# Performance work log

Measured on AMD Instinct MI355X. Metric: run time of the kernel, lower is better.

## Reference

```python
import jax, jax.numpy as jnp
import numpy as np

B, C, F_IN = 262144, 4, 4   # batch, num label nodes, feature dim
HID = 64                     # hidden_dim (MLP embedding dim / GCN input)
GCN_H, GCN_OUT = 32, 4
EPS = 1e-8                   # torch F.cosine_similarity eps


def _glorot(k, shape):
    lim = float(np.sqrt(6.0 / (shape[0] + shape[1])))
    return jax.random.uniform(k, shape, jnp.float32, -lim, lim)


def setup_inputs() -> dict:
    key = jax.random.key(0)
    ks = jax.random.split(key, 7)
    return dict(
        x=jax.random.normal(ks[0], (B, C, F_IN), jnp.float32),
        # LabelEmbeddingMLP: 4 -> 128 -> 64 -> HID
        W1=_glorot(ks[1], (F_IN, 128)), b1=jnp.zeros((128,), jnp.float32),
        W2=_glorot(ks[2], (128, 64)),   b2=jnp.zeros((64,), jnp.float32),
        W3=_glorot(ks[3], (64, HID)),   b3=jnp.zeros((HID,), jnp.float32),
        # GCNModel: GCNConv(HID,32) -> GCNConv(32,4)
        Wg1=_glorot(ks[4], (HID, GCN_H)), bg1=jnp.zeros((GCN_H,), jnp.float32),
        Wg2=_glorot(ks[5], (GCN_H, GCN_OUT)), bg2=jnp.zeros((GCN_OUT,), jnp.float32),
    )


def reference(x, W1, b1, W2, b2, W3, b3, Wg1, bg1, Wg2, bg2):
    # --- label embedding MLP (applied per node) ---
    h = jax.nn.relu(x @ W1 + b1)
    h = jax.nn.relu(h @ W2 + b2)
    emb = h @ W3 + b3                                    # [B, C, HID]

    # --- per-sample cosine similarity, thresholded, unioned over batch ---
    # (the torch code keeps adding edges to ONE nx.Graph across all k, so the
    #  resulting 4-node edge set is the union over the batch; edge weights are
    #  ignored because GCNConv is called without edge_weight)
    n = x / jnp.maximum(jnp.linalg.norm(x, axis=-1, keepdims=True), EPS)
    sim = jnp.einsum('bif,bjf->bij', n, n)               # [B, C, C]
    adj = (sim > 0.5).any(axis=0) & ~jnp.eye(C, dtype=bool)
    adj = adj | adj.T

    # --- GCN normalized adjacency with self-loops: D^-1/2 (A+I) D^-1/2 ---
    A = adj.astype(jnp.float32) + jnp.eye(C, dtype=jnp.float32)
    dinv = jax.lax.rsqrt(A.sum(axis=1))
    Ahat = jax.lax.stop_gradient(dinv[:, None] * A * dinv[None, :])  # graph built via .item() is detached in torch

    # --- two GCNConv layers, shared Ahat broadcast over batch ---
    g = jax.nn.relu(jnp.einsum('ij,bjh->bih', Ahat, emb @ Wg1) + bg1)  # [B, C, 32]
    out = jnp.einsum('ij,bjh->bih', Ahat, g @ Wg2) + bg2               # [B, C, 4]
    return emb, out
```

## Files before the change

### kernel.cpp

```cpp
#include <hip/hip_runtime.h>

#define NB 262144
#define NNODE (NB * 4)
#define EMB_ELEMS ((size_t)NNODE * 64)
#define ADJ_BLOCKS (NNODE / 256)

typedef __attribute__((ext_vector_type(8))) _Float16 f16x8;
typedef __attribute__((ext_vector_type(4))) float f32x4;
typedef __attribute__((ext_vector_type(4))) unsigned int u32x4;

#define OW1E  0
#define OW2T  10240
#define OW3T  27648
#define OW3GT 36864
#define OF32  41472
#define IMG_BYTES 42880
#define FB2   0
#define FB3   64
#define FB3G  128
#define FBG1  160
#define FWG2  192
#define FBG2  320
#define FAHAT 324

#define NWAVE 8
#define SB_STRIDE 36
#define WBUF_BYTES (64 * SB_STRIDE * 2)
#define SMEM_BYTES (IMG_BYTES + NWAVE * WBUF_BYTES)

template <int J>
__device__ __forceinline__ float qb(float v) {
    constexpr int ctrl = J | (J << 2) | (J << 4) | (J << 6);
    int r = __builtin_amdgcn_update_dpp(0, __builtin_bit_cast(int, v), ctrl, 0xF, 0xF, true);
    return __builtin_bit_cast(float, r);
}

__device__ __forceinline__ float sum_xor16(float u) {
    float a = u, b = u;
    asm("v_permlane16_swap_b32 %0, %1" : "+v"(a), "+v"(b));
    return a + b;
}
__device__ __forceinline__ float sum_xor32(float u) {
    float a = u, b = u;
    asm("v_permlane32_swap_b32 %0, %1" : "+v"(a), "+v"(b));
    return a + b;
}

__global__ __launch_bounds__(256) void adj_kernel(const float* __restrict__ x,
                                                  unsigned int* __restrict__ mask_arr) {
    __shared__ unsigned int smask;
    if (threadIdx.x == 0) smask = 0u;
    __syncthreads();

    const int t = blockIdx.x * 256 + threadIdx.x;
    const int c = t & 3;
    f32x4 v = *(const f32x4*)(x + (size_t)t * 4);
    float nn = sqrtf(v.x * v.x + v.y * v.y + v.z * v.z + v.w * v.w);
    float inv = 1.0f / fmaxf(nn, 1e-8f);

    unsigned int m = 0u;
#define DOTJ(J) do {                                                            \
        const float bx = qb<J>(v.x), by = qb<J>(v.y);                           \
        const float bz = qb<J>(v.z), bw = qb<J>(v.w);                           \
        const float bi = qb<J>(inv);                                            \
        const float d = v.x * bx + v.y * by + v.z * bz + v.w * bw;              \
        if ((int)((J) != c) & (int)(d * inv * bi > 0.5f)) {                     \
            const int i_ = c < (J) ? c : (J);                                   \
            const int j_ = c < (J) ? (J) : c;                                   \
            m |= 1u << (2 * i_ + j_ - 1 - (i_ >> 1));                           \
        }                                                                       \
    } while (0)
    DOTJ(0); DOTJ(1); DOTJ(2); DOTJ(3);
#undef DOTJ

    if (m) atomicOr(&smask, m);
    __syncthreads();
    if (threadIdx.x == 0) mask_arr[blockIdx.x] = smask;
}

__global__ __launch_bounds__(256) void prep_kernel(
    const float* __restrict__ W1, const float* __restrict__ b1,
    const float* __restrict__ W2, const float* __restrict__ b2,
    const float* __restrict__ W3, const float* __restrict__ b3,
    const float* __restrict__ Wg1, const float* __restrict__ bg1,
    const float* __restrict__ Wg2, const float* __restrict__ bg2,
    const unsigned int* __restrict__ mask_arr, char* __restrict__ img)
{
    const int t = threadIdx.x;
    const int bid = blockIdx.x;
    _Float16* H = (_Float16*)img;
    float* F = (float*)(img + OF32);

    if (bid == 0) {
        __shared__ unsigned red[256];
        unsigned um = 0u;
        for (int i = t; i < ADJ_BLOCKS; i += 256) um |= mask_arr[i];
        red[t] = um;
        __syncthreads();
        for (int s = 128; s > 0; s >>= 1) {
            if (t < s) red[t] |= red[t + s];
            __syncthreads();
        }
        const unsigned m = red[0];

        for (int i = t; i < 64; i += 256) F[FB2 + i] = b2[i];
        for (int i = t; i < 64; i += 256) F[FB3 + i] = b3[i];
        for (int i = t; i < 32; i += 256) {
            float s = 0.f;
            for (int h = 0; h < 64; ++h) s = fmaf(b3[h], Wg1[h * 32 + i], s);
            F[FB3G + i] = s;
        }
        for (int i = t; i < 32; i += 256) F[FBG1 + i] = bg1[i];
        for (int i = t; i < 128; i += 256) F[FWG2 + i] = Wg2[i];
        for (int i = t; i < 4; i += 256) F[FBG2 + i] = bg2[i];
        if (t == 0) {
            float A[4][4];
            for (int i = 0; i < 4; ++i)
                for (int j = 0; j < 4; ++j) A[i][j] = (i == j) ? 1.f : 0.f;
            int bit = 0;
            for (int i = 0; i < 4; ++i)
                for (int j = i + 1; j < 4; ++j) {
                    if ((m >> bit) & 1u) { A[i][j] = 1.f; A[j][i] = 1.f; }
                    ++bit;
                }
            float dinv[4];
            for (int i = 0; i < 4; ++i)
                dinv[i] = 1.0f / sqrtf(A[i][0] + A[i][1] + A[i][2] + A[i][3]);
            for (int i = 0; i < 4; ++i)
                for (int j = 0; j < 4; ++j) F[FAHAT + i * 4 + j] = dinv[i] * A[i][j] * dinv[j];
        }
    } else if (bid == 1) {
        for (int i = t; i < 128 * 40; i += 256) {
            int j = i / 40, kk = i % 40;
            float v = (kk < 4) ? W1[kk * 128 + j] : (kk == 4 ? b1[j] : 0.f);
            H[OW1E / 2 + i] = (_Float16)v;
        }
    } else if (bid == 2) {
        for (int i = t; i < 64 * 136; i += 256) {
            int jo = i / 136, ji = i % 136;
            H[OW2T / 2 + i] = (_Float16)(ji < 128 ? W2[ji * 64 + jo] : 0.f);
        }
    } else {
        for (int i = t; i < 64 * 72; i += 256) {
            int h = i / 72, j = i % 72;
            H[OW3T / 2 + i] = (_Float16)(j < 64 ? W3[j * 64 + h] : 0.f);
        }
        for (int i = t; i < 32 * 72; i += 256) {
            int e = i / 72, j = i % 72;
            float s = 0.f;
            if (j < 64)
                for (int h = 0; h < 64; ++h) s = fmaf(W3[j * 64 + h], Wg1[h * 32 + e], s);
            H[OW3GT / 2 + i] = (_Float16)s;
        }
    }
}

__device__ __forceinline__ unsigned pkf16(float a, float b) {
    unsigned short ha = __builtin_bit_cast(unsigned short, (_Float16)a);
    unsigned short hb = __builtin_bit_cast(unsigned short, (_Float16)b);
    return (unsigned)ha | ((unsigned)hb << 16);
}
__device__ __forceinline__ f32x4 MF(f16x8 a, f16x8 b, f32x4 c) {
    return __builtin_amdgcn_mfma_f32_16x16x32_f16(a, b, c, 0, 0, 0);
}
__device__ __forceinline__ f16x8 ldA(const _Float16* p) {
    return *(const f16x8*)p;
}

__global__ __launch_bounds__(512, 2) void mlp_gcn_mfma(
    const float* __restrict__ x, const char* __restrict__ img,
    float* __restrict__ emb_out, float* __restrict__ out_out)
{
    __shared__ u32x4 smem4[SMEM_BYTES / 16];
    char* smem = (char*)smem4;
    const int tx = threadIdx.x;
    {
        const u32x4* src = (const u32x4*)img;
        u32x4* dst = (u32x4*)smem;
        for (int i = tx; i < IMG_BYTES / 16; i += 512) dst[i] = src[i];
    }
    __syncthreads();

    const _Float16* wh = (const _Float16*)smem;
    const float* wf = (const float*)(smem + OF32);

    const int wid = tx >> 6, lane = tx & 63;
    const int g = lane >> 4, c = lane & 15;
    const bool g0 = (g == 0);

    char* wb = smem + IMG_BYTES + wid * WBUF_BYTES;
    _Float16* sb = (_Float16*)wb;
    float* tb = (float*)wb;

    const f32x4 arow = *(const f32x4*)(wf + FAHAT + (c & 3) * 4);
    f32x4 bg1v[2];
    bg1v[0] = *(const f32x4*)(wf + FBG1 + g * 4);
    bg1v[1] = *(const f32x4*)(wf + FBG1 + 16 + g * 4);
    const f32x4 bg2v = *(const f32x4*)(wf + FBG2);
    f32x4 wg2v[2][4];
#pragma unroll
    for (int m = 0; m < 2; ++m)
#pragma unroll
        for (int r = 0; r < 4; ++r)
            wg2v[m][r] = *(const f32x4*)(wf + FWG2 + (m * 16 + g * 4 + r) * 4);

    const size_t nbase0 = ((size_t)blockIdx.x * NWAVE + wid) * 128;
    f32x4 xv = *(const f32x4*)(x + (nbase0 + lane) * 4);

#pragma unroll 1
    for (int it = 0; it < 2; ++it) {
        const size_t nbase = nbase0 + (size_t)it * 64;
        const size_t pn = (it < 1) ? (nbase + 64) : nbase;
        f32x4 xnext = *(const f32x4*)(x + (pn + lane) * 4);

        {
            uint2 w0; w0.x = pkf16(xv.x, xv.y); w0.y = pkf16(xv.z, xv.w);
            uint2 w1; w1.x = 0x00003C00u; w1.y = 0u;
            *(uint2*)(sb + lane * SB_STRIDE + 0) = w0;
            *(uint2*)(sb + lane * SB_STRIDE + 4) = w1;
        }
        f16x8 xB[4];
#pragma unroll
        for (int nt = 0; nt < 4; ++nt) {
            uint2 lo = *(const uint2*)(sb + (nt * 16 + c) * SB_STRIDE + 0);
            uint2 hi = *(const uint2*)(sb + (nt * 16 + c) * SB_STRIDE + 4);
            u32x4 t;
            t.x = g0 ? lo.x : 0u; t.y = g0 ? lo.y : 0u;
            t.z = g0 ? hi.x : 0u; t.w = 0u;
            xB[nt] = __builtin_bit_cast(f16x8, t);
        }

        f32x4 acc2[4][4];
#pragma unroll
        for (int mt = 0; mt < 4; ++mt) {
            f32x4 bv = *(const f32x4*)(wf + FB2 + mt * 16 + g * 4);
#pragma unroll
            for (int nt = 0; nt < 4; ++nt) acc2[mt][nt] = bv;
        }
#pragma unroll
        for (int kt = 0; kt < 4; ++kt) {
#pragma unroll
            for (int mt2 = 0; mt2 < 2; ++mt2) {
                const int mt = 2 * kt + mt2;
                f16x8 a = ldA(wh + OW1E / 2 + (mt * 16 + c) * 40 + g * 8);
#pragma unroll
                for (int nt = 0; nt < 4; ++nt) {
                    f32x4 z = {0.f, 0.f, 0.f, 0.f};
                    f32x4 t = MF(a, xB[nt], z);
                    uint2 w;
                    w.x = pkf16(fmaxf(t[0], 0.f), fmaxf(t[1], 0.f));
                    w.y = pkf16(fmaxf(t[2], 0.f), fmaxf(t[3], 0.f));
                    *(uint2*)(sb + (nt * 16 + c) * SB_STRIDE + mt2 * 16 + g * 4) = w;
                }
            }
            f16x8 bf[4];
#pragma unroll
            for (int nt = 0; nt < 4; ++nt) {
                uint2 lo = *(const uint2*)(sb + (nt * 16 + c) * SB_STRIDE + g * 8);
                uint2 hi = *(const uint2*)(sb + (nt * 16 + c) * SB_STRIDE + g * 8 + 4);
                u32x4 t; t.x = lo.x; t.y = lo.y; t.z = hi.x; t.w = hi.y;
                bf[nt] = __builtin_bit_cast(f16x8, t);
            }
#pragma unroll
            for (int mt = 0; mt < 4; ++mt) {
                f16x8 a = ldA(wh + OW2T / 2 + (mt * 16 + c) * 136 + kt * 32 + g * 8);
#pragma unroll
                for (int nt = 0; nt < 4; ++nt) acc2[mt][nt] = MF(a, bf[nt], acc2[mt][nt]);
            }
        }

        unsigned pk2a[4][4][2];
#pragma unroll
        for (int mt = 0; mt < 4; ++mt)
#pragma unroll
            for (int nt = 0; nt < 4; ++nt) {
                pk2a[mt][nt][0] = pkf16(fmaxf(acc2[mt][nt][0], 0.f), fmaxf(acc2[mt][nt][1], 0.f));
                pk2a[mt][nt][1] = pkf16(fmaxf(acc2[mt][nt][2], 0.f), fmaxf(acc2[mt][nt][3], 0.f));
            }

        f32x4 acc3[4][4], acc4[2][4];
#pragma unroll
        for (int mt = 0; mt < 4; ++mt) {
            f32x4 bv = *(const f32x4*)(wf + FB3 + mt * 16 + g * 4);
#pragma unroll
            for (int nt = 0; nt < 4; ++nt) acc3[mt][nt] = bv;
        }
#pragma unroll
        for (int mt = 0; mt < 2; ++mt) {
            f32x4 bv = *(const f32x4*)(wf + FB3G + mt * 16 + g * 4);
#pragma unroll
            for (int nt = 0; nt < 4; ++nt) acc4[mt][nt] = bv;
        }
#pragma unroll
        for (int kt = 0; kt < 2; ++kt) {
#pragma unroll
            for (int mt2 = 0; mt2 < 2; ++mt2) {
                const int mt = 2 * kt + mt2;
#pragma unroll
                for (int nt = 0; nt < 4; ++nt) {
                    uint2 w; w.x = pk2a[mt][nt][0]; w.y = pk2a[mt][nt][1];
                    *(uint2*)(sb + (nt * 16 + c) * SB_STRIDE + mt2 * 16 + g * 4) = w;
                }
            }
            f16x8 bf[4];
#pragma unroll
            for (int nt = 0; nt < 4; ++nt) {
                uint2 lo = *(const uint2*)(sb + (nt * 16 + c) * SB_STRIDE + g * 8);
                uint2 hi = *(const uint2*)(sb + (nt * 16 + c) * SB_STRIDE + g * 8 + 4);
                u32x4 t; t.x = lo.x; t.y = lo.y; t.z = hi.x; t.w = hi.y;
                bf[nt] = __builtin_bit_cast(f16x8, t);
            }
#pragma unroll
            for (int mt = 0; mt < 4; ++mt) {
                f16x8 a = ldA(wh + OW3T / 2 + (mt * 16 + c) * 72 + kt * 32 + g * 8);
#pragma unroll
                for (int nt = 0; nt < 4; ++nt) acc3[mt][nt] = MF(a, bf[nt], acc3[mt][nt]);
            }
#pragma unroll
            for (int mt = 0; mt < 2; ++mt) {
                f16x8 a = ldA(wh + OW3GT / 2 + (mt * 16 + c) * 72 + kt * 32 + g * 8);
#pragma unroll
                for (int nt = 0; nt < 4; ++nt) acc4[mt][nt] = MF(a, bf[nt], acc4[mt][nt]);
            }
        }

#pragma unroll
        for (int nt = 0; nt < 4; ++nt) {
#pragma unroll
            for (int mt = 0; mt < 4; ++mt) {
                int sl = (mt * 4 + g) ^ (c & 7);
                *(f32x4*)(tb + c * 64 + sl * 4) = acc3[mt][nt];
            }
            float* gp = emb_out + (nbase + nt * 16) * 64;
#pragma unroll
            for (int s = 0; s < 4; ++s) {
                int row = s * 4 + g;
                int sl = c ^ (row & 7);
                f32x4 q = *(const f32x4*)(tb + row * 64 + sl * 4);
                *(f32x4*)(gp + s * 256 + lane * 4) = q;
            }
        }

#pragma unroll
        for (int nt = 0; nt < 4; ++nt) {
            float u[4] = {0.f, 0.f, 0.f, 0.f};
#pragma unroll
            for (int m = 0; m < 2; ++m)
#pragma unroll
                for (int r = 0; r < 4; ++r) {
                    float v = acc4[m][nt][r];
                    float s = bg1v[m][r];
                    s = fmaf(arow.x, qb<0>(v), s);
                    s = fmaf(arow.y, qb<1>(v), s);
                    s = fmaf(arow.z, qb<2>(v), s);
                    s = fmaf(arow.w, qb<3>(v), s);
                    s = fmaxf(s, 0.f);
                    u[0] = fmaf(s, wg2v[m][r].x, u[0]);
                    u[1] = fmaf(s, wg2v[m][r].y, u[1]);
                    u[2] = fmaf(s, wg2v[m][r].z, u[2]);
                    u[3] = fmaf(s, wg2v[m][r].w, u[3]);
                }
#pragma unroll
            for (int o = 0; o < 4; ++o)
                u[o] = sum_xor32(sum_xor16(u[o]));
            float ov[4];
#pragma unroll
            for (int o = 0; o < 4; ++o) {
                float s = bg2v[o];
                s = fmaf(arow.x, qb<0>(u[o]), s);
                s = fmaf(arow.y, qb<1>(u[o]), s);
                s = fmaf(arow.z, qb<2>(u[o]), s);
                s = fmaf(arow.w, qb<3>(u[o]), s);
                ov[o] = s;
            }
            if (g0) {
                f32x4 t; t.x = ov[0]; t.y = ov[1]; t.z = ov[2]; t.w = ov[3];
                *(f32x4*)(out_out + (nbase + nt * 16 + c) * 4) = t;
            }
        }

        xv = xnext;
    }
}

extern "C" void kernel_launch(void* const* d_in, const int* in_sizes, int n_in,
                              void* d_out, int out_size, void* d_ws, size_t ws_size,
                              hipStream_t stream) {
    const float* x   = (const float*)d_in[0];
    const float* W1  = (const float*)d_in[1];
    const float* b1  = (const float*)d_in[2];
    const float* W2  = (const float*)d_in[3];
    const float* b2  = (const float*)d_in[4];
    const float* W3  = (const float*)d_in[5];
    const float* b3  = (const float*)d_in[6];
    const float* Wg1 = (const float*)d_in[7];
    const float* bg1 = (const float*)d_in[8];
    const float* Wg2 = (const float*)d_in[9];
    const float* bg2 = (const float*)d_in[10];

    unsigned int* mask_arr = (unsigned int*)d_ws;
    char* img = (char*)d_ws + 16640;

    float* emb_out = (float*)d_out;
    float* out_out = emb_out + EMB_ELEMS;

    adj_kernel<<<ADJ_BLOCKS, 256, 0, stream>>>(x, mask_arr);
    prep_kernel<<<4, 256, 0, stream>>>(W1, b1, W2, b2, W3, b3, Wg1, bg1, Wg2, bg2,
                                       mask_arr, img);
    mlp_gcn_mfma<<<NNODE / 1024, 512, 0, stream>>>(x, img, emb_out, out_out);
}
```

Measured before the change: 118.1 us.

## Permute weight K-order so MFMA outputs feed next MFMA directly in registers

Reorders the K dimension of the W2, W3 and fused W3·Wg1 weight images with a permutation, so that the accumulator layout of one MFMA matches the B-operand layout of the next. The LDS write/read round trip between the layer-1→2 and layer-2→3 stages is then replaced by packing registers straight into operands. The permlane16/32 swap reductions are also replaced with __shfl_xor. This removes LDS traffic and waits, but the generic shuffles may be more costly than the permlane swaps.

```diff
diff --git a/kernel.cpp b/kernel.cpp
--- a/kernel.cpp
+++ b/kernel.cpp
@@ -28,22 +28,16 @@
 #define WBUF_BYTES (64 * SB_STRIDE * 2)
 #define SMEM_BYTES (IMG_BYTES + NWAVE * WBUF_BYTES)
 
+__device__ __forceinline__ int kperm(int ji) {
+    int kt = ji >> 5, r = ji & 31, g = r >> 3, e = r & 7;
+    return kt * 32 + ((e >> 2) << 4) + (g << 2) + (e & 3);
+}
+
 template <int J>
 __device__ __forceinline__ float qb(float v) {
     constexpr int ctrl = J | (J << 2) | (J << 4) | (J << 6);
     int r = __builtin_amdgcn_update_dpp(0, __builtin_bit_cast(int, v), ctrl, 0xF, 0xF, true);
     return __builtin_bit_cast(float, r);
-}
-
-__device__ __forceinline__ float sum_xor16(float u) {
-    float a = u, b = u;
-    asm("v_permlane16_swap_b32 %0, %1" : "+v"(a), "+v"(b));
-    return a + b;
-}
-__device__ __forceinline__ float sum_xor32(float u) {
-    float a = u, b = u;
-    asm("v_permlane32_swap_b32 %0, %1" : "+v"(a), "+v"(b));
-    return a + b;
 }
 
 __global__ __launch_bounds__(256) void adj_kernel(const float* __restrict__ x,
@@ -138,18 +132,24 @@
     } else if (bid == 2) {
         for (int i = t; i < 64 * 136; i += 256) {
             int jo = i / 136, ji = i % 136;
-            H[OW2T / 2 + i] = (_Float16)(ji < 128 ? W2[ji * 64 + jo] : 0.f);
+            float v = 0.f;
+            if (ji < 128) v = W2[kperm(ji) * 64 + jo];
+            H[OW2T / 2 + i] = (_Float16)v;
         }
     } else {
         for (int i = t; i < 64 * 72; i += 256) {
             int h = i / 72, j = i % 72;
-            H[OW3T / 2 + i] = (_Float16)(j < 64 ? W3[j * 64 + h] : 0.f);
+            float v = 0.f;
+            if (j < 64) v = W3[kperm(j) * 64 + h];
+            H[OW3T / 2 + i] = (_Float16)v;
         }
         for (int i = t; i < 32 * 72; i += 256) {
             int e = i / 72, j = i % 72;
             float s = 0.f;
-            if (j < 64)
-                for (int h = 0; h < 64; ++h) s = fmaf(W3[j * 64 + h], Wg1[h * 32 + e], s);
+            if (j < 64) {
+                const int jj = kperm(j);
+                for (int h = 0; h < 64; ++h) s = fmaf(W3[jj * 64 + h], Wg1[h * 32 + e], s);
+            }
             H[OW3GT / 2 + i] = (_Float16)s;
         }
     }
@@ -165,6 +165,11 @@
 }
 __device__ __forceinline__ f16x8 ldA(const _Float16* p) {
     return *(const f16x8*)p;
+}
+__device__ __forceinline__ f16x8 bcat(unsigned X0, unsigned X1,
+                                      unsigned Y0, unsigned Y1) {
+    u32x4 t; t.x = X0; t.y = X1; t.z = Y0; t.w = Y1;
+    return __builtin_bit_cast(f16x8, t);
 }
 
 __global__ __launch_bounds__(512, 2) void mlp_gcn_mfma(
@@ -239,27 +244,18 @@
         }
 #pragma unroll
         for (int kt = 0; kt < 4; ++kt) {
-#pragma unroll
-            for (int mt2 = 0; mt2 < 2; ++mt2) {
-                const int mt = 2 * kt + mt2;
-                f16x8 a = ldA(wh + OW1E / 2 + (mt * 16 + c) * 40 + g * 8);
-#pragma unroll
-                for (int nt = 0; nt < 4; ++nt) {
-                    f32x4 z = {0.f, 0.f, 0.f, 0.f};
-                    f32x4 t = MF(a, xB[nt], z);
-                    uint2 w;
-                    w.x = pkf16(fmaxf(t[0], 0.f), fmaxf(t[1], 0.f));
-                    w.y = pkf16(fmaxf(t[2], 0.f), fmaxf(t[3], 0.f));
-                    *(uint2*)(sb + (nt * 16 + c) * SB_STRIDE + mt2 * 16 + g * 4) = w;
-                }
-            }
+            f16x8 a0 = ldA(wh + OW1E / 2 + ((2 * kt + 0) * 16 + c) * 40 + g * 8);
+            f16x8 a1 = ldA(wh + OW1E / 2 + ((2 * kt + 1) * 16 + c) * 40 + g * 8);
             f16x8 bf[4];
 #pragma unroll
             for (int nt = 0; nt < 4; ++nt) {
-                uint2 lo = *(const uint2*)(sb + (nt * 16 + c) * SB_STRIDE + g * 8);
-                uint2 hi = *(const uint2*)(sb + (nt * 16 + c) * SB_STRIDE + g * 8 + 4);
-                u32x4 t; t.x = lo.x; t.y = lo.y; t.z = hi.x; t.w = hi.y;
-                bf[nt] = __builtin_bit_cast(f16x8, t);
+                f32x4 z = {0.f, 0.f, 0.f, 0.f};
+                f32x4 t0 = MF(a0, xB[nt], z);
+                f32x4 t1 = MF(a1, xB[nt], z);
+                bf[nt] = bcat(pkf16(fmaxf(t0[0], 0.f), fmaxf(t0[1], 0.f)),
+                              pkf16(fmaxf(t0[2], 0.f), fmaxf(t0[3], 0.f)),
+                              pkf16(fmaxf(t1[0], 0.f), fmaxf(t1[1], 0.f)),
+                              pkf16(fmaxf(t1[2], 0.f), fmaxf(t1[3], 0.f)));
             }
 #pragma unroll
             for (int mt = 0; mt < 4; ++mt) {
@@ -293,23 +289,11 @@
         }
 #pragma unroll
         for (int kt = 0; kt < 2; ++kt) {
-#pragma unroll
-            for (int mt2 = 0; mt2 < 2; ++mt2) {
-                const int mt = 2 * kt + mt2;
-#pragma unroll
-                for (int nt = 0; nt < 4; ++nt) {
-                    uint2 w; w.x = pk2a[mt][nt][0]; w.y = pk2a[mt][nt][1];
-                    *(uint2*)(sb + (nt * 16 + c) * SB_STRIDE + mt2 * 16 + g * 4) = w;
-                }
-            }
             f16x8 bf[4];
 #pragma unroll
-            for (int nt = 0; nt < 4; ++nt) {
-                uint2 lo = *(const uint2*)(sb + (nt * 16 + c) * SB_STRIDE + g * 8);
-                uint2 hi = *(const uint2*)(sb + (nt * 16 + c) * SB_STRIDE + g * 8 + 4);
-                u32x4 t; t.x = lo.x; t.y = lo.y; t.z = hi.x; t.w = hi.y;
-                bf[nt] = __builtin_bit_cast(f16x8, t);
-            }
+            for (int nt = 0; nt < 4; ++nt)
+                bf[nt] = bcat(pk2a[2 * kt][nt][0], pk2a[2 * kt][nt][1],
+                              pk2a[2 * kt + 1][nt][0], pk2a[2 * kt + 1][nt][1]);
 #pragma unroll
             for (int mt = 0; mt < 4; ++mt) {
                 f16x8 a = ldA(wh + OW3T / 2 + (mt * 16 + c) * 72 + kt * 32 + g * 8);
@@ -361,8 +345,10 @@
                     u[3] = fmaf(s, wg2v[m][r].w, u[3]);
                 }
 #pragma unroll
-            for (int o = 0; o < 4; ++o)
-                u[o] = sum_xor32(sum_xor16(u[o]));
+            for (int o = 0; o < 4; ++o) {
+                u[o] += __shfl_xor(u[o], 16);
+                u[o] += __shfl_xor(u[o], 32);
+            }
             float ov[4];
 #pragma unroll
             for (int o = 0; o < 4; ++o) {
```

Result: faster. 112.8 us (-4.5%).
